# Kernel tuning notes

Measured on AMD Instinct MI355X. Metric: run time of the kernel, lower is better.

The kernel has to match this reference:

```python
import jax, jax.numpy as jnp
import numpy as np

# dims matching init_kwargs
M   = 8      # VMD_K components
S   = 1     # seq per component (forced to 1 by shape consistency)
DIN = 1024   # input_size (= d_k = d_v in MHA)
H   = 4      # n_head
HID = 1024   # hidden_size (= d_o)
KSZ = 4096   # Kernel_size (codebook rows)
DK, DV = DIN, DIN
D = HID * M  # codeword dimension


def setup_inputs() -> dict:
    key = jax.random.key(0)
    ks = jax.random.split(key, 13)
    w = lambda i, shape: jax.random.normal(ks[i], shape, jnp.float32) * 0.02
    return {
        "x":    jax.random.normal(ks[0], (M, S, DIN), jnp.float32),
        # per-component MHA params (torch Linear layout: [out, in])
        "Wq": w(1, (M, H * DK, DIN)), "bq": w(2, (M, H * DK)),
        "Wk": w(3, (M, H * DK, DIN)), "bk": w(4, (M, H * DK)),
        "Wv": w(5, (M, H * DV, DIN)), "bv": w(6, (M, H * DV)),
        "Wo": w(7, (M, HID, H * DV)), "bo": w(8, (M, HID)),
        # codebook params (torch.rand -> uniform[0,1))
        "K": jax.random.uniform(ks[9], (KSZ, D), jnp.float32),
        "W": jax.random.uniform(ks[10], (D,), jnp.float32),
        # final Linear(D, 1)
        "Wout": w(11, (1, D)), "bout": w(12, (1,)),
    }


def reference(x, Wq, bq, Wk, bk, Wv, bv, Wo, bo, K, W, Wout, bout):
    # --- per-component multi-head self-attention, vectorized over M ---
    def split_heads(t, dh):  # [M,S,H*dh] -> [M,H,S,dh]
        return t.reshape(M, S, H, dh).transpose(0, 2, 1, 3)

    q = split_heads(jnp.einsum('msd,mod->mso', x, Wq) + bq[:, None, :], DK)
    k = split_heads(jnp.einsum('msd,mod->mso', x, Wk) + bk[:, None, :], DK)
    v = split_heads(jnp.einsum('msd,mod->mso', x, Wv) + bv[:, None, :], DV)
    scale = jnp.sqrt(jnp.float32(DK))
    attn = jax.nn.softmax(jnp.einsum('mhsd,mhtd->mhst', q, k) / scale, axis=-1)
    o = jnp.einsum('mhst,mhtd->mhsd', attn, v)            # [M,H,S,DV]
    o = o.transpose(0, 2, 1, 3).reshape(M, S, H * DV)     # concat heads
    out = (jnp.einsum('msd,mod->mso', o, Wo) + bo[:, None, :]).reshape(-1)  # [D]

    # --- weighted L2 distance to every codeword ---
    dis_feature = (out[None, :] - K) * W[None, :]         # [KSZ, D]
    # faithful to original: dis[i] = sum over the WHOLE buffer after filling
    # rows 0..i (rows >i still zero)  ==>  cumulative sum of row norms
    dis = jnp.cumsum(jnp.sum(dis_feature * dis_feature, axis=1))  # [KSZ]
    index = jnp.argmin(dis)
    sel = dis_feature[index] * W                          # [D]
    return jax.nn.sigmoid(sel @ Wout.T + bout)            # [1]
```

## Files before the change

kernel.cpp:

```cpp
#include <hip/hip_runtime.h>
#include <math.h>

#define M_COMP 8
#define DIN    1024
#define HDV    4096
#define HID    1024
#define DTOT   8192

__device__ __forceinline__ float wave_reduce_sum(float v) {
    #pragma unroll
    for (int off = 32; off > 0; off >>= 1)
        v += __shfl_down(v, off, 64);
    return v;
}

__global__ __launch_bounds__(256) void k_v_matvec(
    const float* __restrict__ x, const float* __restrict__ Wv,
    const float* __restrict__ bv, float* __restrict__ v_out)
{
    const int gwave = (int)((blockIdx.x * blockDim.x + threadIdx.x) >> 6);
    const int lane  = threadIdx.x & 63;
    if (gwave >= M_COMP * HDV) return;
    const int m = gwave >> 12;
    const float* __restrict__ xr = x + m * DIN;
    const float* __restrict__ wr = Wv + (size_t)gwave * DIN;
    float acc = 0.f;
    #pragma unroll
    for (int it = 0; it < DIN / 256; ++it) {
        const int d = it * 256 + lane * 4;
        const float4 w4 = *reinterpret_cast<const float4*>(wr + d);
        const float4 x4 = *reinterpret_cast<const float4*>(xr + d);
        acc += w4.x * x4.x + w4.y * x4.y + w4.z * x4.z + w4.w * x4.w;
    }
    acc = wave_reduce_sum(acc);
    if (lane == 0) v_out[gwave] = acc + bv[gwave];
}

__global__ __launch_bounds__(256) void k_out_matvec(
    const float* __restrict__ v, const float* __restrict__ Wo,
    const float* __restrict__ bo, const float* __restrict__ K0,
    const float* __restrict__ W, const float* __restrict__ Wout,
    float* __restrict__ t_out)
{
    const int d    = (int)((blockIdx.x * blockDim.x + threadIdx.x) >> 6);
    const int lane = threadIdx.x & 63;
    if (d >= DTOT) return;
    const int m = d >> 10;
    const float* __restrict__ vr = v + m * HDV;
    const float* __restrict__ wr = Wo + (size_t)d * HDV;
    float acc = 0.f;
    #pragma unroll
    for (int it = 0; it < HDV / 256; ++it) {
        const int i = it * 256 + lane * 4;
        const float4 w4 = *reinterpret_cast<const float4*>(wr + i);
        const float4 v4 = *reinterpret_cast<const float4*>(vr + i);
        acc += w4.x * v4.x + w4.y * v4.y + w4.z * v4.z + w4.w * v4.w;
    }
    acc = wave_reduce_sum(acc);
    if (lane == 0) {
        const float outd = acc + bo[d];
        const float w    = W[d];
        t_out[d] = (outd - K0[d]) * w * w * Wout[d];
    }
}

__global__ __launch_bounds__(256) void k_final(
    const float* __restrict__ t, const float* __restrict__ bout,
    float* __restrict__ out)
{
    __shared__ float sred[4];
    const int tid = threadIdx.x;
    float acc = 0.f;
    #pragma unroll
    for (int k = 0; k < DTOT / 256; ++k)
        acc += t[tid + k * 256];
    acc = wave_reduce_sum(acc);
    if ((tid & 63) == 0) sred[tid >> 6] = acc;
    __syncthreads();
    if (tid == 0) {
        const float total = sred[0] + sred[1] + sred[2] + sred[3] + bout[0];
        out[0] = 1.f / (1.f + expf(-total));
    }
}

extern "C" void kernel_launch(void* const* d_in, const int* in_sizes, int n_in,
                              void* d_out, int out_size, void* d_ws, size_t ws_size,
                              hipStream_t stream) {
    const float* x    = (const float*)d_in[0];
    const float* Wv   = (const float*)d_in[5];
    const float* bv   = (const float*)d_in[6];
    const float* Wo   = (const float*)d_in[7];
    const float* bo   = (const float*)d_in[8];
    const float* K    = (const float*)d_in[9];
    const float* W    = (const float*)d_in[10];
    const float* Wout = (const float*)d_in[11];
    const float* bout = (const float*)d_in[12];
    float* out = (float*)d_out;

    float* v_ws = (float*)d_ws;
    float* t_ws = v_ws + (M_COMP * HDV);

    k_v_matvec<<<(M_COMP * HDV) / 4, 256, 0, stream>>>(x, Wv, bv, v_ws);
    k_out_matvec<<<DTOT / 4, 256, 0, stream>>>(v_ws, Wo, bo, K, W, Wout, t_ws);
    k_final<<<1, 256, 0, stream>>>(t_ws, bout, out);
}
```

Baseline: 48.25 us.

## Reassociate output projection to overlap Wo streaming with Wv matvec in one kernel

The final scalar is rewritten as dot(v, u), where u = Wo^T·(W²·Wout). This removes the dependency of the Wo pass on v, so the Wo column-weighted reduction can run in the same launch as the Wv matvec, interleaved block by block. Partial u vectors go to workspace, and a combine kernel forms the dot product with v plus the bias term. The change adds workspace traffic and a partial-count choice based on ws_size, and uses nontemporal loads on the weight streams.

```diff
diff --git a/kernel.cpp b/kernel.cpp
--- a/kernel.cpp
+++ b/kernel.cpp
@@ -1,11 +1,15 @@
 #include <hip/hip_runtime.h>
 #include <math.h>
 
-#define M_COMP 8
-#define DIN    1024
-#define HDV    4096
-#define HID    1024
-#define DTOT   8192
+#define M_COMP  8
+#define DIN     1024
+#define HDV     4096
+#define HID     1024
+#define DTOT    8192
+#define NV_ROWS 32768
+#define V_BLOCKS 8192
+
+typedef float f32x4 __attribute__((ext_vector_type(4)));
 
 __device__ __forceinline__ float wave_reduce_sum(float v) {
     #pragma unroll
@@ -14,13 +18,102 @@
     return v;
 }
 
+__global__ __launch_bounds__(256) void k_fused(
+    const float* __restrict__ x, const float* __restrict__ Wv,
+    const float* __restrict__ bv, const float* __restrict__ Wo,
+    const float* __restrict__ W, const float* __restrict__ Wout,
+    float* __restrict__ v_out, float* __restrict__ upart,
+    int npart, int stride, int J)
+{
+    const int bid  = blockIdx.x;
+    const int bq   = bid / stride;
+    const int lane = threadIdx.x & 63;
+    const int wib  = threadIdx.x >> 6;
+
+    if ((bid % stride) != 0) {
+        const int vb  = bid - bq - 1;
+        const int row = vb * 4 + wib;
+        const int m   = row >> 12;
+        const float* __restrict__ xr = x + m * DIN;
+        const float* __restrict__ wr = Wv + (size_t)row * DIN;
+        float acc = 0.f;
+        #pragma unroll
+        for (int it = 0; it < DIN / 256; ++it) {
+            const int d = it * 256 + lane * 4;
+            const f32x4 w4 = __builtin_nontemporal_load(
+                reinterpret_cast<const f32x4*>(wr + d));
+            const f32x4 x4 = *reinterpret_cast<const f32x4*>(xr + d);
+            acc += w4.x * x4.x + w4.y * x4.y + w4.z * x4.z + w4.w * x4.w;
+        }
+        acc = wave_reduce_sum(acc);
+        if (lane == 0) v_out[row] = acc + bv[row];
+    } else {
+        const int w     = bq * 4 + wib;
+        const int per_m = 16 * npart;
+        const int m     = w / per_m;
+        const int rem   = w % per_m;
+        const int ic    = rem / npart;
+        const int jc    = rem % npart;
+        const int d0    = m * HID + jc * J;
+        const float* __restrict__ base =
+            Wo + (size_t)d0 * HDV + ic * 256 + lane * 4;
+        f32x4 acc = {0.f, 0.f, 0.f, 0.f};
+        #pragma unroll 4
+        for (int j = 0; j < J; ++j) {
+            const float wj = W[d0 + j];
+            const float c  = wj * wj * Wout[d0 + j];
+            const f32x4 w4 = __builtin_nontemporal_load(
+                reinterpret_cast<const f32x4*>(base + (size_t)j * HDV));
+            acc += w4 * c;
+        }
+        *reinterpret_cast<f32x4*>(
+            upart + (size_t)jc * NV_ROWS + m * HDV + ic * 256 + lane * 4) = acc;
+    }
+}
+
+__global__ __launch_bounds__(256) void k_combine(
+    const float* __restrict__ v, const float* __restrict__ upart, int npart,
+    const float* __restrict__ bo, const float* __restrict__ K0,
+    const float* __restrict__ W, const float* __restrict__ Wout,
+    float* __restrict__ partials)
+{
+    const int b = blockIdx.x, t = threadIdx.x;
+    const int e = b * 256 + t;
+    float u = 0.f;
+    for (int p = 0; p < npart; ++p) u += upart[(size_t)p * NV_ROWS + e];
+    float val = u * v[e];
+    if (t < 64) {
+        const int d = b * 64 + t;
+        const float w = W[d];
+        val += (bo[d] - K0[d]) * w * w * Wout[d];
+    }
+    val = wave_reduce_sum(val);
+    __shared__ float s[4];
+    if ((t & 63) == 0) s[t >> 6] = val;
+    __syncthreads();
+    if (t == 0) partials[b] = s[0] + s[1] + s[2] + s[3];
+}
+
+__global__ __launch_bounds__(128) void k_final2(
+    const float* __restrict__ partials, const float* __restrict__ bout,
+    float* __restrict__ out)
+{
+    const int t = threadIdx.x;
+    float val = partials[t];
+    val = wave_reduce_sum(val);
+    __shared__ float s[2];
+    if ((t & 63) == 0) s[t >> 6] = val;
+    __syncthreads();
+    if (t == 0) out[0] = 1.f / (1.f + expf(-(s[0] + s[1] + bout[0])));
+}
+
 __global__ __launch_bounds__(256) void k_v_matvec(
     const float* __restrict__ x, const float* __restrict__ Wv,
     const float* __restrict__ bv, float* __restrict__ v_out)
 {
     const int gwave = (int)((blockIdx.x * blockDim.x + threadIdx.x) >> 6);
     const int lane  = threadIdx.x & 63;
-    if (gwave >= M_COMP * HDV) return;
+    if (gwave >= NV_ROWS) return;
     const int m = gwave >> 12;
     const float* __restrict__ xr = x + m * DIN;
     const float* __restrict__ wr = Wv + (size_t)gwave * DIN;
@@ -98,9 +191,32 @@
     float* out = (float*)d_out;
 
     float* v_ws = (float*)d_ws;
-    float* t_ws = v_ws + (M_COMP * HDV);
-
-    k_v_matvec<<<(M_COMP * HDV) / 4, 256, 0, stream>>>(x, Wv, bv, v_ws);
-    k_out_matvec<<<DTOT / 4, 256, 0, stream>>>(v_ws, Wo, bo, K, W, Wout, t_ws);
-    k_final<<<1, 256, 0, stream>>>(t_ws, bout, out);
-}
+
+    const size_t base_need = ((size_t)NV_ROWS + 128) * sizeof(float);
+    int npart = 0;
+    const int cands[5] = {32, 16, 8, 4, 2};
+    for (int i = 0; i < 5; ++i) {
+        if (ws_size >= base_need + (size_t)cands[i] * NV_ROWS * sizeof(float)) {
+            npart = cands[i];
+            break;
+        }
+    }
+
+    if (npart) {
+        float* upart    = v_ws + NV_ROWS;
+        float* partials = upart + (size_t)npart * NV_ROWS;
+        const int stride = 256 / npart + 1;
+        const int total  = V_BLOCKS + 32 * npart;
+        const int J      = HID / npart;
+        k_fused<<<total, 256, 0, stream>>>(x, Wv, bv, Wo, W, Wout,
+                                           v_ws, upart, npart, stride, J);
+        k_combine<<<128, 256, 0, stream>>>(v_ws, upart, npart, bo, K, W, Wout,
+                                           partials);
+        k_final2<<<1, 128, 0, stream>>>(partials, bout, out);
+    } else {
+        float* t_ws = v_ws + NV_ROWS;
+        k_v_matvec<<<NV_ROWS / 4, 256, 0, stream>>>(x, Wv, bv, v_ws);
+        k_out_matvec<<<DTOT / 4, 256, 0, stream>>>(v_ws, Wo, bo, K, W, Wout, t_ws);
+        k_final<<<1, 256, 0, stream>>>(t_ws, bout, out);
+    }
+}
```

Result: slower. 61.41 us (+27.3%).
